# Kernel tuning notes

Hardware: AMD Instinct MI355X
Metric: run time of the kernel (lower is better)

The kernel has to match this reference:

```python
import jax, jax.numpy as jnp
import numpy as np

N, D, K = 131072, 64, 1024
EPS = 1e-05
INIT_BOUND = 1.0 / 256


def setup_inputs() -> dict:
    key = jax.random.key(0)
    k1, k2 = jax.random.split(key)
    x_flat = jax.random.normal(k1, (N, D), dtype=jnp.float32)
    embedding = jax.random.uniform(k2, (K, D), dtype=jnp.float32,
                                   minval=-INIT_BOUND, maxval=INIT_BOUND)
    return {"it": 1, "x_flat": x_flat, "embedding": embedding}


def reference(it, x_flat, embedding):
    # it != 0 path: use existing codebook (iter==0 random-sample init is a
    # data-shuffling side effect, excluded from the kernel-pattern reference).
    k = embedding.shape[0]
    # distances[n,k] = ||e_k||^2 + ||x_n||^2 - 2 x_n . e_k   (addmm pattern)
    distances = (jnp.sum(embedding ** 2, axis=1)
                 + jnp.sum(x_flat ** 2, axis=1, keepdims=True)
                 - 2.0 * (x_flat @ embedding.T))
    indices = jnp.argmin(distances.astype(jnp.float32), axis=-1)  # [N]

    # distortion = mse(x, embedding[indices])
    quantized = embedding[indices]                                 # [N,D] gather
    cluster_distortion = jnp.mean((x_flat - quantized) ** 2)

    # codebook update: one-hot matmuls are exactly segment sums
    ema_count = jax.ops.segment_sum(jnp.ones((x_flat.shape[0],), x_flat.dtype),
                                    indices, num_segments=k)       # [K]
    n = jnp.sum(ema_count)
    ema_count = (ema_count + EPS) / (n + k * EPS) * n
    ema_weight = jax.ops.segment_sum(x_flat, indices, num_segments=k)  # [K,D]
    new_embedding = ema_weight / ema_count[:, None]

    return cluster_distortion, new_embedding, ema_count
```

## Files before the change

### kernel.cpp

```cpp
#include <hip/hip_runtime.h>

#define NPTS 131072
#define DIM 64
#define KC 1024
#define TK 128
#define BLK 256

__global__ void enorm_kernel(const float* __restrict__ emb, float* __restrict__ enorm) {
    int k = blockIdx.x * blockDim.x + threadIdx.x;
    if (k < KC) {
        const float4* e = (const float4*)(emb + (size_t)k * DIM);
        float s = 0.f;
#pragma unroll
        for (int j = 0; j < DIM / 4; ++j) {
            float4 v = e[j];
            s += v.x * v.x + v.y * v.y + v.z * v.z + v.w * v.w;
        }
        enorm[k] = s;
    }
}

__global__ __launch_bounds__(BLK) void assign_kernel(
    const float* __restrict__ x, const float* __restrict__ emb,
    const float* __restrict__ enorm,
    float* __restrict__ count, float* __restrict__ weight,
    double* __restrict__ dacc)
{
    __shared__ float4 eT[TK * (DIM / 4)];
    __shared__ float  eN[TK];
    __shared__ float  wsum[BLK / 64];

    const int tid = threadIdx.x;
    const int pt  = blockIdx.x * BLK + tid;

    float4 xr[DIM / 4];
    const float4* xp = (const float4*)(x + (size_t)pt * DIM);
#pragma unroll
    for (int j = 0; j < DIM / 4; ++j) xr[j] = xp[j];

    float best  = 3.4e38f;
    int   bestk = 0;

    for (int t = 0; t < KC / TK; ++t) {
        __syncthreads();
        const float4* ep = (const float4*)(emb + (size_t)t * TK * DIM);
#pragma unroll
        for (int j = 0; j < (TK * DIM / 4) / BLK; ++j)
            eT[j * BLK + tid] = ep[j * BLK + tid];
        if (tid < TK) eN[tid] = enorm[t * TK + tid];
        __syncthreads();

        for (int k = 0; k < TK; ++k) {
            const float4* ek = &eT[k * (DIM / 4)];
            float d0 = 0.f, d1 = 0.f, d2 = 0.f, d3 = 0.f;
#pragma unroll
            for (int j = 0; j < DIM / 4; ++j) {
                float4 e4 = ek[j];
                d0 = fmaf(xr[j].x, e4.x, d0);
                d1 = fmaf(xr[j].y, e4.y, d1);
                d2 = fmaf(xr[j].z, e4.z, d2);
                d3 = fmaf(xr[j].w, e4.w, d3);
            }
            float s = fmaf(-2.f, (d0 + d1) + (d2 + d3), eN[k]);
            if (s < best) { best = s; bestk = t * TK + k; }
        }
    }

    float xn = 0.f;
#pragma unroll
    for (int j = 0; j < DIM / 4; ++j)
        xn += xr[j].x * xr[j].x + xr[j].y * xr[j].y + xr[j].z * xr[j].z + xr[j].w * xr[j].w;
    float dloc = xn + best;

#pragma unroll
    for (int off = 32; off > 0; off >>= 1) dloc += __shfl_down(dloc, off, 64);
    if ((tid & 63) == 0) wsum[tid >> 6] = dloc;
    __syncthreads();
    if (tid == 0) {
        float b = wsum[0] + wsum[1] + wsum[2] + wsum[3];
        atomicAdd(dacc, (double)b);
    }

    unsafeAtomicAdd(&count[bestk], 1.0f);
    float* w = weight + (size_t)bestk * DIM;
#pragma unroll
    for (int j = 0; j < DIM / 4; ++j) {
        unsafeAtomicAdd(&w[4 * j + 0], xr[j].x);
        unsafeAtomicAdd(&w[4 * j + 1], xr[j].y);
        unsafeAtomicAdd(&w[4 * j + 2], xr[j].z);
        unsafeAtomicAdd(&w[4 * j + 3], xr[j].w);
    }
}

__global__ void finalize_kernel(const float* __restrict__ count,
                                const float* __restrict__ weight,
                                const double* __restrict__ dacc,
                                float* __restrict__ out)
{
    int idx = blockIdx.x * BLK + threadIdx.x;
    const float denomf = (float)(131072.0 + (double)KC * 1.0e-5);
    if (idx < KC * DIM) {
        int k = idx >> 6;
        float cn = (count[k] + 1e-5f) / denomf * 131072.0f;
        out[1 + idx] = weight[idx] / cn;
    } else if (idx < KC * DIM + KC) {
        int k = idx - KC * DIM;
        float cn = (count[k] + 1e-5f) / denomf * 131072.0f;
        out[1 + KC * DIM + k] = cn;
    } else if (idx == KC * DIM + KC) {
        out[0] = (float)(*dacc * (1.0 / ((double)NPTS * (double)DIM)));
    }
}

extern "C" void kernel_launch(void* const* d_in, const int* in_sizes, int n_in,
                              void* d_out, int out_size, void* d_ws, size_t ws_size,
                              hipStream_t stream)
{
    const float* x   = (const float*)d_in[1];
    const float* emb = (const float*)d_in[2];
    float* out = (float*)d_out;

    float*  enorm  = (float*)d_ws;
    float*  count  = enorm + KC;
    float*  weight = count + KC;
    size_t  daccOff = (size_t)(2 * KC + KC * DIM) * sizeof(float);
    double* dacc   = (double*)((char*)d_ws + daccOff);

    hipMemsetAsync(d_ws, 0, daccOff + sizeof(double), stream);

    enorm_kernel<<<(KC + BLK - 1) / BLK, BLK, 0, stream>>>(emb, enorm);
    assign_kernel<<<NPTS / BLK, BLK, 0, stream>>>(x, emb, enorm, count, weight, dacc);

    int fin_elems = KC * DIM + KC + 1;
    finalize_kernel<<<(fin_elems + BLK - 1) / BLK, BLK, 0, stream>>>(count, weight, dacc, out);
}
```

Before: 1.231 ms.

## Register-tile the distance GEMM with 8x8 per-thread blocks and shared x tile

Replaces the one-point-per-thread distance loop with a register-blocked tile: each block loads 128 points and 128 codes per pass into transposed shared memory, and each thread computes an 8x8 set of dot products. This raises arithmetic intensity, since each shared load now feeds 8 FMAs instead of one. Argmin is reduced across lanes with shuffles and then across waves through shared memory, with index tie-breaking. The scatter atomics are split so two threads handle the halves of each point. The costs are higher register pressure (64 accumulators plus operands) that may lower occupancy, and twice as many blocks.

```diff
diff --git a/kernel.cpp b/kernel.cpp
--- a/kernel.cpp
+++ b/kernel.cpp
@@ -3,8 +3,11 @@
 #define NPTS 131072
 #define DIM 64
 #define KC 1024
-#define TK 128
 #define BLK 256
+#define MT 128
+#define NT 128
+#define NPASS (KC / NT)
+#define DC 16
 
 __global__ void enorm_kernel(const float* __restrict__ emb, float* __restrict__ enorm) {
     int k = blockIdx.x * blockDim.x + threadIdx.x;
@@ -12,7 +15,7 @@
         const float4* e = (const float4*)(emb + (size_t)k * DIM);
         float s = 0.f;
 #pragma unroll
-        for (int j = 0; j < DIM / 4; ++j) {
+        for (int j = 0; j < DC; ++j) {
             float4 v = e[j];
             s += v.x * v.x + v.y * v.y + v.z * v.z + v.w * v.w;
         }
@@ -26,69 +29,143 @@
     float* __restrict__ count, float* __restrict__ weight,
     double* __restrict__ dacc)
 {
-    __shared__ float4 eT[TK * (DIM / 4)];
-    __shared__ float  eN[TK];
-    __shared__ float  wsum[BLK / 64];
-
-    const int tid = threadIdx.x;
-    const int pt  = blockIdx.x * BLK + tid;
-
-    float4 xr[DIM / 4];
-    const float4* xp = (const float4*)(x + (size_t)pt * DIM);
-#pragma unroll
-    for (int j = 0; j < DIM / 4; ++j) xr[j] = xp[j];
-
-    float best  = 3.4e38f;
-    int   bestk = 0;
-
-    for (int t = 0; t < KC / TK; ++t) {
+    __shared__ float4 xT[DC * MT];
+    __shared__ float4 eT[DC * NT];
+    __shared__ float  bvL[2][MT];
+    __shared__ int    bcL[2][MT];
+    __shared__ float  xnL[MT];
+    __shared__ float  wsum[4];
+
+    const int tid  = threadIdx.x;
+    const int lane = tid & 63;
+    const int wid  = tid >> 6;
+    const int wm   = wid >> 1;
+    const int wn   = wid & 1;
+    const int kc   = lane & 7;
+    const int pr   = lane >> 3;
+    const size_t pblock = (size_t)blockIdx.x * MT;
+
+    {
+        const float4* xg = (const float4*)(x + pblock * DIM);
+#pragma unroll
+        for (int s = 0; s < (DC * MT) / BLK; ++s) {
+            int g = s * BLK + tid;
+            int p = g >> 4, dc = g & 15;
+            xT[dc * MT + p] = xg[g];
+        }
+    }
+
+    float bv[8], xn[8];
+    int   bc[8];
+#pragma unroll
+    for (int i = 0; i < 8; ++i) { bv[i] = 3.4e38f; bc[i] = 0; xn[i] = 0.f; }
+
+    for (int pass = 0; pass < NPASS; ++pass) {
         __syncthreads();
-        const float4* ep = (const float4*)(emb + (size_t)t * TK * DIM);
-#pragma unroll
-        for (int j = 0; j < (TK * DIM / 4) / BLK; ++j)
-            eT[j * BLK + tid] = ep[j * BLK + tid];
-        if (tid < TK) eN[tid] = enorm[t * TK + tid];
+        const float4* eg = (const float4*)(emb + (size_t)pass * NT * DIM);
+#pragma unroll
+        for (int s = 0; s < (DC * NT) / BLK; ++s) {
+            int g = s * BLK + tid;
+            int c = g >> 4, dc = g & 15;
+            eT[dc * NT + c] = eg[g];
+        }
         __syncthreads();
 
-        for (int k = 0; k < TK; ++k) {
-            const float4* ek = &eT[k * (DIM / 4)];
-            float d0 = 0.f, d1 = 0.f, d2 = 0.f, d3 = 0.f;
-#pragma unroll
-            for (int j = 0; j < DIM / 4; ++j) {
-                float4 e4 = ek[j];
-                d0 = fmaf(xr[j].x, e4.x, d0);
-                d1 = fmaf(xr[j].y, e4.y, d1);
-                d2 = fmaf(xr[j].z, e4.z, d2);
-                d3 = fmaf(xr[j].w, e4.w, d3);
+        float eNr[8];
+#pragma unroll
+        for (int j = 0; j < 8; ++j) eNr[j] = enorm[pass * NT + wn * 64 + 8 * j + kc];
+
+        float acc[8][8];
+#pragma unroll
+        for (int i = 0; i < 8; ++i)
+#pragma unroll
+            for (int j = 0; j < 8; ++j) acc[i][j] = 0.f;
+
+#pragma unroll
+        for (int dc = 0; dc < DC; ++dc) {
+            float4 a[8], b[8];
+#pragma unroll
+            for (int i = 0; i < 8; ++i) a[i] = xT[dc * MT + wm * 64 + 8 * i + pr];
+#pragma unroll
+            for (int j = 0; j < 8; ++j) b[j] = eT[dc * NT + wn * 64 + 8 * j + kc];
+#pragma unroll
+            for (int i = 0; i < 8; ++i)
+#pragma unroll
+                for (int j = 0; j < 8; ++j) {
+                    acc[i][j] = fmaf(a[i].x, b[j].x, acc[i][j]);
+                    acc[i][j] = fmaf(a[i].y, b[j].y, acc[i][j]);
+                    acc[i][j] = fmaf(a[i].z, b[j].z, acc[i][j]);
+                    acc[i][j] = fmaf(a[i].w, b[j].w, acc[i][j]);
+                }
+            if (pass == 0) {
+#pragma unroll
+                for (int i = 0; i < 8; ++i) {
+                    xn[i] = fmaf(a[i].x, a[i].x, xn[i]);
+                    xn[i] = fmaf(a[i].y, a[i].y, xn[i]);
+                    xn[i] = fmaf(a[i].z, a[i].z, xn[i]);
+                    xn[i] = fmaf(a[i].w, a[i].w, xn[i]);
+                }
             }
-            float s = fmaf(-2.f, (d0 + d1) + (d2 + d3), eN[k]);
-            if (s < best) { best = s; bestk = t * TK + k; }
-        }
-    }
-
-    float xn = 0.f;
-#pragma unroll
-    for (int j = 0; j < DIM / 4; ++j)
-        xn += xr[j].x * xr[j].x + xr[j].y * xr[j].y + xr[j].z * xr[j].z + xr[j].w * xr[j].w;
-    float dloc = xn + best;
-
-#pragma unroll
-    for (int off = 32; off > 0; off >>= 1) dloc += __shfl_down(dloc, off, 64);
-    if ((tid & 63) == 0) wsum[tid >> 6] = dloc;
+        }
+
+        const int cbase = pass * NT + wn * 64 + kc;
+#pragma unroll
+        for (int i = 0; i < 8; ++i)
+#pragma unroll
+            for (int j = 0; j < 8; ++j) {
+                float s = fmaf(-2.f, acc[i][j], eNr[j]);
+                int   c = cbase + 8 * j;
+                if (s < bv[i] || (s == bv[i] && c < bc[i])) { bv[i] = s; bc[i] = c; }
+            }
+    }
+
+#pragma unroll
+    for (int i = 0; i < 8; ++i) {
+#pragma unroll
+        for (int m = 1; m < 8; m <<= 1) {
+            float ov = __shfl_xor(bv[i], m, 64);
+            int   oc = __shfl_xor(bc[i], m, 64);
+            if (ov < bv[i] || (ov == bv[i] && oc < bc[i])) { bv[i] = ov; bc[i] = oc; }
+        }
+    }
+
+    if (kc == 0) {
+#pragma unroll
+        for (int i = 0; i < 8; ++i) {
+            int p = wm * 64 + 8 * i + pr;
+            bvL[wn][p] = bv[i];
+            bcL[wn][p] = bc[i];
+            if (wn == 0) xnL[p] = xn[i];
+        }
+    }
     __syncthreads();
-    if (tid == 0) {
-        float b = wsum[0] + wsum[1] + wsum[2] + wsum[3];
-        atomicAdd(dacc, (double)b);
-    }
-
-    unsafeAtomicAdd(&count[bestk], 1.0f);
-    float* w = weight + (size_t)bestk * DIM;
-#pragma unroll
-    for (int j = 0; j < DIM / 4; ++j) {
-        unsafeAtomicAdd(&w[4 * j + 0], xr[j].x);
-        unsafeAtomicAdd(&w[4 * j + 1], xr[j].y);
-        unsafeAtomicAdd(&w[4 * j + 2], xr[j].z);
-        unsafeAtomicAdd(&w[4 * j + 3], xr[j].w);
+
+    const int p  = tid >> 1;
+    const int hf = tid & 1;
+    float bvp = bvL[0][p];
+    int   bcp = bcL[0][p];
+    {
+        float ov = bvL[1][p];
+        int   oc = bcL[1][p];
+        if (ov < bvp || (ov == bvp && oc < bcp)) { bvp = ov; bcp = oc; }
+    }
+    float dloc = (hf == 0) ? (xnL[p] + bvp) : 0.f;
+
+#pragma unroll
+    for (int off = 32; off; off >>= 1) dloc += __shfl_down(dloc, off, 64);
+    if (lane == 0) wsum[wid] = dloc;
+    __syncthreads();
+    if (tid == 0) atomicAdd(dacc, (double)(wsum[0] + wsum[1] + wsum[2] + wsum[3]));
+
+    if (hf == 0) unsafeAtomicAdd(&count[bcp], 1.0f);
+    float* w = weight + (size_t)bcp * DIM + hf * 32;
+#pragma unroll
+    for (int dc = 0; dc < 8; ++dc) {
+        float4 v = xT[(hf * 8 + dc) * MT + p];
+        unsafeAtomicAdd(&w[4 * dc + 0], v.x);
+        unsafeAtomicAdd(&w[4 * dc + 1], v.y);
+        unsafeAtomicAdd(&w[4 * dc + 2], v.z);
+        unsafeAtomicAdd(&w[4 * dc + 3], v.w);
     }
 }
 
@@ -129,7 +206,7 @@
     hipMemsetAsync(d_ws, 0, daccOff + sizeof(double), stream);
 
     enorm_kernel<<<(KC + BLK - 1) / BLK, BLK, 0, stream>>>(emb, enorm);
-    assign_kernel<<<NPTS / BLK, BLK, 0, stream>>>(x, emb, enorm, count, weight, dacc);
+    assign_kernel<<<NPTS / MT, BLK, 0, stream>>>(x, emb, enorm, count, weight, dacc);
 
     int fin_elems = KC * DIM + KC + 1;
     finalize_kernel<<<(fin_elems + BLK - 1) / BLK, BLK, 0, stream>>>(count, weight, dacc, out);
```

Result: slower. 2.420 ms (+96.6%).
